# Optimization experiments

Hardware: AMD Instinct MI355X
Metric: run time of the kernel (lower is better)

## Reference

```python
import jax, jax.numpy as jnp
import numpy as np

BETA = 0.25  # commitment weight per level (vqconfig default)
EPS = 1e-12  # F.normalize eps


def setup_inputs() -> dict:
    key = jax.random.key(0)
    k1, k2 = jax.random.split(key)
    z = jax.random.normal(k1, (4, 256, 32, 32), dtype=jnp.float32)
    cb = jax.random.normal(k2, (4, 4096, 256), dtype=jnp.float32)
    # embeddings are row-normalized at init in the torch module
    cb = cb / jnp.maximum(jnp.linalg.norm(cb, axis=-1, keepdims=True), EPS)
    return {"z": z, "codebooks": cb}


def _nearest_code(r_flat, embed):
    """use_znorm=True path: cosine-similarity nearest neighbor.
    r_flat: (N, C), embed: (K, C) -> idx: (N,) int32"""
    rn = r_flat / jnp.maximum(jnp.linalg.norm(r_flat, axis=1, keepdims=True), EPS)
    en = embed / jnp.maximum(jnp.linalg.norm(embed, axis=1, keepdims=True), EPS)
    sim = jnp.einsum('nc,kc->nk', rn, en)  # (N, K)
    return jnp.argmax(sim, axis=1)


def reference(z, codebooks):
    """Residual VQ over L codebooks (eval mode: no EMA / kmeans init).
    z: (B, C, H, W); codebooks: (L, K, C).
    Returns (z_q_st (B,C,H,W), indices (L,B,H,W), qloss scalar)."""
    B, C, H, W = z.shape
    L = codebooks.shape[0]
    z_flat = z.transpose(0, 2, 3, 1).reshape(-1, C)  # (N, C)
    residual = z_flat
    q_sum = jnp.zeros_like(z_flat)
    qloss = jnp.zeros((), dtype=z.dtype)
    indices = []
    for l in range(L):  # small fixed level loop with sequential data dependency
        E = codebooks[l]
        idx = _nearest_code(residual, E)          # (N,)
        z_q = E[idx]                              # gather (N, C)
        q_sum = q_sum + z_q
        qloss = qloss + BETA * jnp.mean((jax.lax.stop_gradient(z_q) - residual) ** 2)
        residual = residual - jax.lax.stop_gradient(z_q)
        indices.append(idx.reshape(B, H, W))
    q = q_sum.reshape(B, H, W, C).transpose(0, 3, 1, 2)
    z_q_st = z + jax.lax.stop_gradient(q - z)     # straight-through estimator
    return z_q_st, jnp.stack(indices, axis=0), qloss
```

## Files before the change

### kernel.cpp

```cpp
#include <hip/hip_runtime.h>


#define OFF_AS   0
#define OFF_BS   524288
#define OFF_R    2621440
#define OFF_INV  3670016
#define OFF_CSLC 3686400
#define OFF_CAND 3719168
#define OFF_CVAL 5816320
#define OFF_SSQ  7913472

#define BETA 0.25f
#define EPSN 1e-12f
#define SLC 16
#define MARGIN 0.012f
#define NEGINF -3.0e38f

typedef __attribute__((ext_vector_type(8))) short short8;
typedef __attribute__((ext_vector_type(4))) short short4v;
typedef __attribute__((ext_vector_type(4))) float f32x4;

__device__ __forceinline__ unsigned short f2bf(float x) {
  unsigned u = __float_as_uint(x);
  unsigned r = (u + 0x7fffu + ((u >> 16) & 1u)) >> 16;
  return (unsigned short)r;
}

__device__ __forceinline__ void gload16(const void* g, void* s) {
  __builtin_amdgcn_global_load_lds(
      (const __attribute__((address_space(1))) unsigned int*)g,
      (__attribute__((address_space(3))) unsigned int*)s, 16, 0, 0);
}

__global__ __launch_bounds__(256) void k_prep(const float* __restrict__ z,
                                              const float* __restrict__ cb,
                                              float* __restrict__ r,
                                              unsigned short* __restrict__ AS,
                                              float* __restrict__ rnorm,
                                              float* __restrict__ inv,
                                              unsigned short* __restrict__ BS) {
  __shared__ __align__(16) char psm[9472];
  int tid = threadIdx.x;
  int w = tid >> 6, lane = tid & 63;
  if (blockIdx.x < 2048) {
    float (*t)[260] = (float(*)[260])psm;
    float* sinvs = (float*)(psm + 8320);
    int r0 = blockIdx.x * 8;
#pragma unroll
    for (int p = 0; p < 2; ++p) {
      int idx = p * 1024 + tid * 4;
      float4 v = *(const float4*)(cb + (size_t)r0 * 256 + idx);
      int row = idx >> 8, c = idx & 255;
      *(float4*)&t[row][c] = v;
    }
    __syncthreads();
#pragma unroll
    for (int rr = 0; rr < 2; ++rr) {
      int row = w * 2 + rr;
      float4 v = *(const float4*)&t[row][lane * 4];
      float s = v.x * v.x + v.y * v.y + v.z * v.z + v.w * v.w;
#pragma unroll
      for (int off = 32; off; off >>= 1) s += __shfl_xor(s, off);
      if (lane == 0) sinvs[row] = 1.0f / fmaxf(sqrtf(s), EPSN);
    }
    __syncthreads();
    if (tid < 8) inv[r0 + tid] = sinvs[tid];
#pragma unroll
    for (int p = 0; p < 2; ++p) {
      int idx = p * 1024 + tid * 4;
      int row = idx >> 8, c = idx & 255;
      float sc = sinvs[row];
      short4v s4;
      s4[0] = (short)f2bf(t[row][c + 0] * sc);
      s4[1] = (short)f2bf(t[row][c + 1] * sc);
      s4[2] = (short)f2bf(t[row][c + 2] * sc);
      s4[3] = (short)f2bf(t[row][c + 3] * sc);
      *(short4v*)(BS + (size_t)r0 * 256 + idx) = s4;
    }
  } else {
    float (*t)[9] = (float(*)[9])psm;
    float* wpart = (float*)(psm + 9216);
    int n0 = (blockIdx.x - 2048) * 8;
    int b = n0 >> 10, hw0 = n0 & 1023;
#pragma unroll
    for (int p = 0; p < 8; ++p) {
      int c = p * 32 + (tid >> 3), h = tid & 7;
      t[c][h] = z[((b * 256 + c) << 10) + hw0 + h];
    }
    __syncthreads();
#pragma unroll
    for (int h = 0; h < 8; ++h) {
      float v = t[tid][h];
      float s = v * v;
#pragma unroll
      for (int off = 32; off; off >>= 1) s += __shfl_xor(s, off);
      if (lane == 0) wpart[w * 8 + h] = s;
    }
    __syncthreads();
    if (tid < 8) {
      float tot = (wpart[0 * 8 + tid] + wpart[1 * 8 + tid]) +
                  (wpart[2 * 8 + tid] + wpart[3 * 8 + tid]);
      rnorm[n0 + tid] = sqrtf(tot);
    }
#pragma unroll
    for (int h = 0; h < 8; ++h) {
      float v = t[tid][h];
      r[(n0 + h) * 256 + tid] = v;
      AS[(n0 + h) * 256 + tid] = f2bf(v);
    }
  }
}

__global__ __launch_bounds__(256) void k_gemm_argmax(
    const unsigned short* __restrict__ AS, const unsigned short* __restrict__ BS,
    const float* __restrict__ rnorm, unsigned char* __restrict__ cslc,
    int* __restrict__ cand, float* __restrict__ cval) {
  __shared__ __align__(16) char sm[32768];
  unsigned short* lA = (unsigned short*)sm;
  unsigned short* lB = (unsigned short*)(sm + 16384);
  float* sv    = (float*)sm;
  float* scomb = (float*)(sm + 1024);
  float* rn_s  = (float*)(sm + 1536);
  int*   lcnt  = (int*)(sm + 2048);
  int*   lck   = (int*)(sm + 2560);
  float* lcv   = (float*)(sm + 10752);

  int bid = blockIdx.x;
  int wg = (bid & 7) * 128 + (bid >> 3);
  int bm = wg >> 5, bn = wg & 31;
  int mbase = bm * 128, nbase = bn * 128;
  int tid = threadIdx.x;
  int wid = tid >> 6, ln = tid & 63;
  int wr = wid >> 1, wc = wid & 1;
  int grp = ln >> 4, li = ln & 15;

  f32x4 acc[4][4];
#pragma unroll
  for (int i = 0; i < 4; ++i)
#pragma unroll
    for (int j = 0; j < 4; ++j) acc[i][j] = (f32x4){0.f, 0.f, 0.f, 0.f};

  for (int ks = 0; ks < 4; ++ks) {
    __syncthreads();
    int k0 = ks * 64;
#pragma unroll
    for (int i = 0; i < 4; ++i) {
      int idx = i * 256 + tid;
      int row = idx >> 3, cc = idx & 7;
      int src = cc ^ (row & 7);
      gload16(AS + ((mbase + row) << 8) + k0 + src * 8, ((char*)lA) + idx * 16);
    }
#pragma unroll
    for (int i = 0; i < 4; ++i) {
      int idx = i * 256 + tid;
      int row = idx >> 3, cc = idx & 7;
      int src = cc ^ (row & 7);
      gload16(BS + ((nbase + row) << 8) + k0 + src * 8, ((char*)lB) + idx * 16);
    }
    __syncthreads();
#pragma unroll
    for (int kk = 0; kk < 2; ++kk) {
      short8 b[4];
#pragma unroll
      for (int ni = 0; ni < 4; ++ni) {
        int row = wc * 64 + ni * 16 + li;
        int cc = kk * 4 + grp;
        b[ni] = *(const short8*)(((const char*)lB) + row * 128 + (cc ^ (row & 7)) * 16);
      }
#pragma unroll
      for (int mi = 0; mi < 4; ++mi) {
        int row = wr * 64 + mi * 16 + li;
        int cc = kk * 4 + grp;
        short8 a = *(const short8*)(((const char*)lA) + row * 128 + (cc ^ (row & 7)) * 16);
#pragma unroll
        for (int ni = 0; ni < 4; ++ni)
          acc[mi][ni] = __builtin_amdgcn_mfma_f32_16x16x32_bf16(a, b[ni], acc[mi][ni], 0, 0, 0);
      }
    }
  }

  float redv[4][4];
#pragma unroll
  for (int mi = 0; mi < 4; ++mi) {
#pragma unroll
    for (int reg = 0; reg < 4; ++reg) {
      float v = acc[mi][0][reg];
#pragma unroll
      for (int ni = 1; ni < 4; ++ni) v = fmaxf(v, acc[mi][ni][reg]);
#pragma unroll
      for (int off = 1; off < 16; off <<= 1) v = fmaxf(v, __shfl_xor(v, off));
      redv[mi][reg] = v;
    }
  }
  __syncthreads();
#pragma unroll
  for (int mi = 0; mi < 4; ++mi)
#pragma unroll
    for (int reg = 0; reg < 4; ++reg)
      if (li == 0) sv[(wr * 2 + wc) * 64 + mi * 16 + grp * 4 + reg] = redv[mi][reg];
  __syncthreads();
  if (tid < 128) {
    int wr2 = tid >> 6, r64 = tid & 63;
    float m = fmaxf(sv[(wr2 * 2 + 0) * 64 + r64], sv[(wr2 * 2 + 1) * 64 + r64]);
    int n = mbase + wr2 * 64 + r64;
    scomb[wr2 * 64 + r64] = m;
    rn_s[wr2 * 64 + r64] = rnorm[n];
    lcnt[tid] = 0;
  }
  __syncthreads();
#pragma unroll
  for (int mi = 0; mi < 4; ++mi) {
#pragma unroll
    for (int reg = 0; reg < 4; ++reg) {
      int rl = mi * 16 + grp * 4 + reg;
      float thr = scomb[wr * 64 + rl] - MARGIN * rn_s[wr * 64 + rl];
      int rloc = wr * 64 + rl;
#pragma unroll
      for (int ni = 0; ni < 4; ++ni) {
        float v = acc[mi][ni][reg];
        if (v >= thr) {
          int pos = atomicAdd(&lcnt[rloc], 1);
          if (pos < SLC) {
            lck[rloc * SLC + pos] = nbase + wc * 64 + ni * 16 + li;
            lcv[rloc * SLC + pos] = v;
          }
        }
      }
    }
  }
  __syncthreads();
  if (tid < 128) {
    int rloc = tid;
    int n = mbase + rloc;
    int raw = lcnt[rloc];
    int lc = raw < SLC ? raw : SLC;
    cslc[(n << 5) + bn] = (unsigned char)(raw > SLC ? 255 : lc);
    int base = (n << 9) + bn * SLC;
    for (int j = 0; j < lc; ++j) {
      cand[base + j] = lck[rloc * SLC + j];
      cval[base + j] = lcv[rloc * SLC + j];
    }
  }
}

__global__ __launch_bounds__(256) void k_refine_update(
    const float* __restrict__ cb, const float* __restrict__ inv,
    float* __restrict__ r, float* __restrict__ rnorm,
    const unsigned char* __restrict__ cslc,
    const int* __restrict__ cand, const float* __restrict__ cval,
    unsigned short* __restrict__ AS, float* __restrict__ ssq,
    float* __restrict__ out_idx, int l) {
  __shared__ int lists[4][128];
  __shared__ int lcnts[4];
  int tid = threadIdx.x, w = tid >> 6, lane = tid & 63;
  int n = blockIdx.x * 4 + w;
  const float* cbl = cb + ((size_t)l << 20);
  const float* invl = inv + (l << 12);

  float4 rv4 = *(const float4*)(r + ((size_t)n << 8) + lane * 4);

  int cnt_l = cslc[(n << 5) + (lane >> 1)];
  bool ovf = __any(cnt_l == 255);
  int sbase = (n << 9) + (lane >> 1) * 16 + (lane & 1) * 8;
  int4 k0 = *(const int4*)(cand + sbase);
  int4 k1 = *(const int4*)(cand + sbase + 4);
  float4 v0 = *(const float4*)(cval + sbase);
  float4 v1 = *(const float4*)(cval + sbase + 4);
  int nvalid = cnt_l - ((lane & 1) << 3);
  nvalid = nvalid < 0 ? 0 : (nvalid > 8 ? 8 : nvalid);
  float vv[8] = {v0.x, v0.y, v0.z, v0.w, v1.x, v1.y, v1.z, v1.w};
  int   kk[8] = {k0.x, k0.y, k0.z, k0.w, k1.x, k1.y, k1.z, k1.w};

  float gm = NEGINF;
#pragma unroll
  for (int j = 0; j < 8; ++j) if (j < nvalid) gm = fmaxf(gm, vv[j]);
#pragma unroll
  for (int off = 32; off; off >>= 1) gm = fmaxf(gm, __shfl_xor(gm, off));

  float bv = NEGINF; int bk = 0x7fffffff;
  bool full = ovf;
  if (!ovf) {
    float thr = gm - MARGIN * rnorm[n];
    if (lane == 0) lcnts[w] = 0;
#pragma unroll
    for (int j = 0; j < 8; ++j) {
      if (j < nvalid && vv[j] >= thr) {
        int p = atomicAdd(&lcnts[w], 1);
        if (p < 128) lists[w][p] = kk[j];
      }
    }
    int m = lcnts[w];
    if (m <= 128) {
      for (int j = 0; j < m; ++j) {
        int k = lists[w][j];
        float4 e4 = *(const float4*)(cbl + ((size_t)k << 8) + lane * 4);
        float p = rv4.x * e4.x + rv4.y * e4.y + rv4.z * e4.z + rv4.w * e4.w;
#pragma unroll
        for (int off = 32; off; off >>= 1) p += __shfl_xor(p, off);
        float s = p * invl[k];
        if (s > bv || (s == bv && k < bk)) { bv = s; bk = k; }
      }
    } else full = true;
  }
  if (full) {
    bv = NEGINF; bk = 0x7fffffff;
    for (int k = 0; k < 4096; ++k) {
      float4 e4 = *(const float4*)(cbl + ((size_t)k << 8) + lane * 4);
      float p = rv4.x * e4.x + rv4.y * e4.y + rv4.z * e4.z + rv4.w * e4.w;
#pragma unroll
      for (int off = 32; off; off >>= 1) p += __shfl_xor(p, off);
      float s = p * invl[k];
      if (s > bv || (s == bv && k < bk)) { bv = s; bk = k; }
    }
  }
  if (lane == 0) out_idx[(l << 12) + n] = (float)bk;

  float4 e4 = *(const float4*)(cbl + ((size_t)bk << 8) + lane * 4);
  float4 nv = {rv4.x - e4.x, rv4.y - e4.y, rv4.z - e4.z, rv4.w - e4.w};
  *(float4*)(r + ((size_t)n << 8) + lane * 4) = nv;
  if (l != 3) {
    short4v s4;
    s4[0] = (short)f2bf(nv.x); s4[1] = (short)f2bf(nv.y);
    s4[2] = (short)f2bf(nv.z); s4[3] = (short)f2bf(nv.w);
    *(short4v*)(AS + ((size_t)n << 8) + lane * 4) = s4;
  }
  float sq = nv.x * nv.x + nv.y * nv.y + nv.z * nv.z + nv.w * nv.w;
#pragma unroll
  for (int off = 32; off; off >>= 1) sq += __shfl_xor(sq, off);
  if (lane == 0) {
    ssq[(l << 12) + n] = sq;
    if (l != 3) rnorm[n] = sqrtf(sq);
  }
}

__global__ __launch_bounds__(256) void k_writeq_qloss(const float* __restrict__ z,
                                                      const float* __restrict__ r,
                                                      const float* __restrict__ ssq,
                                                      float* __restrict__ out) {
  int tid = threadIdx.x;
  if (blockIdx.x == 1024) {
    __shared__ float wsumq[4];
    float q = 0.f;
    for (int l = 0; l < 4; ++l) {
      float p = 0.f;
#pragma unroll
      for (int i = 0; i < 16; ++i) p += ssq[l * 4096 + i * 256 + tid];
      int lane = tid & 63, w = tid >> 6;
#pragma unroll
      for (int off = 32; off; off >>= 1) p += __shfl_xor(p, off);
      if (lane == 0) wsumq[w] = p;
      __syncthreads();
      float tot = (wsumq[0] + wsumq[1]) + (wsumq[2] + wsumq[3]);
      q += BETA * (tot * (1.0f / (4096.0f * 256.0f)));
      __syncthreads();
    }
    if (tid == 0) out[1048576 + 16384] = q;
    return;
  }
  __shared__ float t[32][33];
  int id = blockIdx.x;
  int b = id >> 8; int rem = id & 255; int ct = rem >> 5; int ht = rem & 31;
  int c0 = ct * 32, h0 = ht * 32;
  int col = tid & 31, row0 = tid >> 5;
#pragma unroll
  for (int p = 0; p < 4; ++p) {
    int row = row0 + p * 8;
    t[row][col] = r[(b * 1024 + h0 + row) * 256 + c0 + col];
  }
  __syncthreads();
#pragma unroll
  for (int p = 0; p < 4; ++p) {
    int row = row0 + p * 8;
    int o = ((b * 256 + c0 + row) << 10) + h0 + col;
    out[o] = z[o] - t[col][row];
  }
}

extern "C" void kernel_launch(void* const* d_in, const int* in_sizes, int n_in,
                              void* d_out, int out_size, void* d_ws, size_t ws_size,
                              hipStream_t stream) {
  const float* z  = (const float*)d_in[0];
  const float* cb = (const float*)d_in[1];
  float* out = (float*)d_out;
  float* ws  = (float*)d_ws;

  unsigned short* AS = (unsigned short*)(ws + OFF_AS);
  unsigned short* BS = (unsigned short*)(ws + OFF_BS);
  float* r     = ws + OFF_R;
  float* inv   = ws + OFF_INV;
  unsigned char* cslc = (unsigned char*)(ws + OFF_CSLC);
  int*   cand  = (int*)(ws + OFF_CAND);
  float* cval  = ws + OFF_CVAL;
  float* ssq   = ws + OFF_SSQ;
  float* rnorm = ws + OFF_SSQ + 16384;

  k_prep<<<2560, 256, 0, stream>>>(z, cb, r, AS, rnorm, inv, BS);
  for (int l = 0; l < 4; ++l) {
    k_gemm_argmax<<<1024, 256, 0, stream>>>(AS, BS + (size_t)l * 4096 * 256,
                                            rnorm, cslc, cand, cval);
    k_refine_update<<<1024, 256, 0, stream>>>(cb, inv, r, rnorm, cslc,
                                              cand, cval, AS, ssq,
                                              out + 1048576, l);
  }
  k_writeq_qloss<<<1025, 256, 0, stream>>>(z, r, ssq, out);
}
```

Before: 166.3 us.

## Double-buffer GEMM K-slices in LDS to overlap global loads with MFMA

The GEMM-argmax kernel's main loop changes from four 64-wide K steps with a single LDS buffer to eight 32-wide K steps using two LDS buffers. The next slice is staged while MFMAs run on the current one, and one barrier per step replaces two. The aim is to hide global-to-LDS load latency behind compute, at the cost of a new XOR swizzle for 64-byte rows and twice as many loop iterations. Whether gload16 is asynchronous (direct-to-LDS) decides how much actually overlaps.

```diff
diff --git a/kernel.cpp b/kernel.cpp
--- a/kernel.cpp
+++ b/kernel.cpp
@@ -116,8 +116,6 @@
     const float* __restrict__ rnorm, unsigned char* __restrict__ cslc,
     int* __restrict__ cand, float* __restrict__ cval) {
   __shared__ __align__(16) char sm[32768];
-  unsigned short* lA = (unsigned short*)sm;
-  unsigned short* lB = (unsigned short*)(sm + 16384);
   float* sv    = (float*)sm;
   float* scomb = (float*)(sm + 1024);
   float* rn_s  = (float*)(sm + 1536);
@@ -140,42 +138,44 @@
 #pragma unroll
     for (int j = 0; j < 4; ++j) acc[i][j] = (f32x4){0.f, 0.f, 0.f, 0.f};
 
-  for (int ks = 0; ks < 4; ++ks) {
+#define STAGE32(SRC, RB, K0, DST)                                              \
+  {                                                                            \
+    _Pragma("unroll")                                                          \
+    for (int i_ = 0; i_ < 2; ++i_) {                                           \
+      int idx_ = i_ * 256 + tid;                                               \
+      int row_ = idx_ >> 2, cc_ = idx_ & 3;                                    \
+      int scc_ = cc_ ^ ((row_ >> 1) & 3);                                      \
+      gload16((SRC) + (((RB) + row_) << 8) + (K0) + scc_ * 8,                  \
+              (DST) + idx_ * 16);                                              \
+    }                                                                          \
+  }
+
+  STAGE32(AS, mbase, 0, sm);
+  STAGE32(BS, nbase, 0, sm + 8192);
+  for (int t = 0; t < 8; ++t) {
     __syncthreads();
-    int k0 = ks * 64;
-#pragma unroll
-    for (int i = 0; i < 4; ++i) {
-      int idx = i * 256 + tid;
-      int row = idx >> 3, cc = idx & 7;
-      int src = cc ^ (row & 7);
-      gload16(AS + ((mbase + row) << 8) + k0 + src * 8, ((char*)lA) + idx * 16);
-    }
-#pragma unroll
-    for (int i = 0; i < 4; ++i) {
-      int idx = i * 256 + tid;
-      int row = idx >> 3, cc = idx & 7;
-      int src = cc ^ (row & 7);
-      gload16(BS + ((nbase + row) << 8) + k0 + src * 8, ((char*)lB) + idx * 16);
-    }
-    __syncthreads();
-#pragma unroll
-    for (int kk = 0; kk < 2; ++kk) {
-      short8 b[4];
-#pragma unroll
-      for (int ni = 0; ni < 4; ++ni) {
-        int row = wc * 64 + ni * 16 + li;
-        int cc = kk * 4 + grp;
-        b[ni] = *(const short8*)(((const char*)lB) + row * 128 + (cc ^ (row & 7)) * 16);
-      }
-#pragma unroll
-      for (int mi = 0; mi < 4; ++mi) {
-        int row = wr * 64 + mi * 16 + li;
-        int cc = kk * 4 + grp;
-        short8 a = *(const short8*)(((const char*)lA) + row * 128 + (cc ^ (row & 7)) * 16);
-#pragma unroll
-        for (int ni = 0; ni < 4; ++ni)
-          acc[mi][ni] = __builtin_amdgcn_mfma_f32_16x16x32_bf16(a, b[ni], acc[mi][ni], 0, 0, 0);
-      }
+    char* cur = sm + (t & 1) * 16384;
+    if (t < 7) {
+      char* nxt = sm + ((t + 1) & 1) * 16384;
+      int k0 = (t + 1) * 32;
+      STAGE32(AS, mbase, k0, nxt);
+      STAGE32(BS, nbase, k0, nxt + 8192);
+    }
+    const char* cA = cur;
+    const char* cB = cur + 8192;
+    short8 b[4];
+#pragma unroll
+    for (int ni = 0; ni < 4; ++ni) {
+      int row = wc * 64 + ni * 16 + li;
+      b[ni] = *(const short8*)(cB + row * 64 + ((grp ^ ((row >> 1) & 3)) * 16));
+    }
+#pragma unroll
+    for (int mi = 0; mi < 4; ++mi) {
+      int row = wr * 64 + mi * 16 + li;
+      short8 a = *(const short8*)(cA + row * 64 + ((grp ^ ((row >> 1) & 3)) * 16));
+#pragma unroll
+      for (int ni = 0; ni < 4; ++ni)
+        acc[mi][ni] = __builtin_amdgcn_mfma_f32_16x16x32_bf16(a, b[ni], acc[mi][ni], 0, 0, 0);
     }
   }
 
@@ -241,6 +241,7 @@
       cval[base + j] = lcv[rloc * SLC + j];
     }
   }
+#undef STAGE32
 }
 
 __global__ __launch_bounds__(256) void k_refine_update(
```

After: 168.8 us. About the same (+1.5%).
